# Kernel tuning notes

Hardware: AMD Instinct MI355X
Metric: run time of the kernel (lower is better)

Reference implementation:

```python
import jax, jax.numpy as jnp
import numpy as np

LN_EPS = 1e-5

def _layernorm(x):
    # LayerNorm over last dim, no affine params (elementwise_affine=False)
    mu = jnp.mean(x, axis=-1, keepdims=True)
    var = jnp.var(x, axis=-1, keepdims=True)
    return (x - mu) / jnp.sqrt(var + LN_EPS)

def setup_inputs() -> dict:
    key = jax.random.key(0)
    k1, k2 = jax.random.split(key)
    B, S, D_IN, D_OUT = 4, 2048, 4096, 4096
    x = jax.random.normal(k1, (B, S, D_IN), dtype=jnp.float32)
    # kaiming-uniform-ish init scale (exact distribution irrelevant for correctness baseline)
    bound = 1.0 / np.sqrt(D_IN)
    weight = jax.random.uniform(k2, (D_OUT, D_IN), dtype=jnp.float32, minval=-bound, maxval=bound)
    return {"x": x, "weight": weight}

def reference(x, weight):
    # weight mean-centering and scalar scale beta
    w_centered = weight - jnp.mean(weight)
    beta = jnp.mean(jnp.abs(w_centered))
    x_norm = _layernorm(x)
    w_bin = jnp.sign(w_centered)                       # [D_out, D_in] in {-1,0,+1}
    out = jnp.einsum('bsi,oi->bso', x_norm, w_bin)     # dense GEMM on binarized weights
    return out * beta
```

## Files before the change

### kernel.cpp

```cpp
#include <hip/hip_runtime.h>
#include <hip/hip_bf16.h>
#include <stdint.h>


typedef __bf16 bf16x8 __attribute__((ext_vector_type(8)));
typedef float f32x4 __attribute__((ext_vector_type(4)));

#define BM 128
#define BN 128
#define BK 32


__device__ __forceinline__ void gl_lds16(const void* g, void* l) {
  __builtin_amdgcn_global_load_lds(
      (const __attribute__((address_space(1))) void*)g,
      (__attribute__((address_space(3))) void*)l,
      16, 0, 0);
}

__device__ __forceinline__ unsigned short f2bf_rne(float f) {
  unsigned int u = __float_as_uint(f);
  unsigned int r = (u + 0x7FFFu + ((u >> 16) & 1u)) >> 16;
  return (unsigned short)r;
}

__device__ __forceinline__ float wave_red(float v) {
#pragma unroll
  for (int o = 32; o > 0; o >>= 1) v += __shfl_down(v, o, 64);
  return v;
}

__device__ __forceinline__ float block_red(float v) {
  __shared__ float tmp[4];
  const int wave = threadIdx.x >> 6, lane = threadIdx.x & 63;
  v = wave_red(v);
  if (lane == 0) tmp[wave] = v;
  __syncthreads();
  float r = 0.f;
  if (threadIdx.x == 0) r = tmp[0] + tmp[1] + tmp[2] + tmp[3];
  return r;
}


__global__ void zero_kernel(float* p) {
  if (threadIdx.x < 8) p[threadIdx.x] = 0.f;
}

__global__ __launch_bounds__(256) void wsum_kernel(const float* __restrict__ w,
                                                   float* __restrict__ scal, int n4) {
  int idx = blockIdx.x * 256 + threadIdx.x;
  int stride = gridDim.x * 256;
  const float4* w4 = (const float4*)w;
  float s = 0.f;
  for (int i = idx; i < n4; i += stride) {
    float4 a = w4[i];
    s += a.x + a.y + a.z + a.w;
  }
  float tot = block_red(s);
  if (threadIdx.x == 0) atomicAdd(&scal[0], tot);
}

__global__ __launch_bounds__(256) void wbin_kernel(const float* __restrict__ w,
                                                   float* __restrict__ scal,
                                                   unsigned short* __restrict__ wb,
                                                   int n4, float inv_n) {
  const float mean = scal[0] * inv_n;
  int idx = blockIdx.x * 256 + threadIdx.x;
  int stride = gridDim.x * 256;
  const float4* w4 = (const float4*)w;
  ushort4* wb4 = (ushort4*)wb;
  float sa = 0.f;
  for (int i = idx; i < n4; i += stride) {
    float4 a = w4[i];
    float dx = a.x - mean, dy = a.y - mean, dz = a.z - mean, dw = a.w - mean;
    sa += fabsf(dx) + fabsf(dy) + fabsf(dz) + fabsf(dw);
    ushort4 o;
    o.x = dx > 0.f ? 0x3F80u : (dx < 0.f ? 0xBF80u : 0u);
    o.y = dy > 0.f ? 0x3F80u : (dy < 0.f ? 0xBF80u : 0u);
    o.z = dz > 0.f ? 0x3F80u : (dz < 0.f ? 0xBF80u : 0u);
    o.w = dw > 0.f ? 0x3F80u : (dw < 0.f ? 0xBF80u : 0u);
    wb4[i] = o;
  }
  float tot = block_red(sa);
  if (threadIdx.x == 0) atomicAdd(&scal[1], tot);
}

__global__ __launch_bounds__(256) void ln_kernel(const float* __restrict__ x,
                                                 __bf16* __restrict__ xn) {
  const int row = blockIdx.x;
  const float4* xr = (const float4*)(x + (size_t)row * 4096);
  const int tid = threadIdx.x;
  float4 v[4];
  float s = 0.f, ss = 0.f;
#pragma unroll
  for (int t = 0; t < 4; t++) {
    float4 a = xr[t * 256 + tid];
    v[t] = a;
    s += a.x + a.y + a.z + a.w;
    ss += a.x * a.x + a.y * a.y + a.z * a.z + a.w * a.w;
  }
#pragma unroll
  for (int o = 32; o > 0; o >>= 1) {
    s += __shfl_down(s, o, 64);
    ss += __shfl_down(ss, o, 64);
  }
  __shared__ float rs[8];
  const int wave = tid >> 6, lane = tid & 63;
  if (lane == 0) { rs[wave] = s; rs[4 + wave] = ss; }
  __syncthreads();
  s = rs[0] + rs[1] + rs[2] + rs[3];
  ss = rs[4] + rs[5] + rs[6] + rs[7];
  const float mu = s * (1.0f / 4096.0f);
  const float var = ss * (1.0f / 4096.0f) - mu * mu;
  const float rstd = rsqrtf(var + 1e-5f);
  ushort4* xw = (ushort4*)((unsigned short*)xn + (size_t)row * 4096);
#pragma unroll
  for (int t = 0; t < 4; t++) {
    float4 a = v[t];
    ushort4 o;
    o.x = f2bf_rne((a.x - mu) * rstd);
    o.y = f2bf_rne((a.y - mu) * rstd);
    o.z = f2bf_rne((a.z - mu) * rstd);
    o.w = f2bf_rne((a.w - mu) * rstd);
    xw[t * 256 + tid] = o;
  }
}

__global__ __launch_bounds__(256) void gemm_kernel(const __bf16* __restrict__ A,
                                                   const __bf16* __restrict__ Bm,
                                                   float* __restrict__ C,
                                                   const float* __restrict__ scal,
                                                   float beta_scale,
                                                   int M, int N, int K) {
  __shared__ __align__(16) __bf16 sA[BM * BK];
  __shared__ __align__(16) __bf16 sB[BN * BK];

  const int tid = threadIdx.x;
  const int wave = tid >> 6;
  const int lane = tid & 63;

  const int rowBase = blockIdx.x * BM;
  const int colBase = blockIdx.y * BN;

  const float beta = scal[1] * beta_scale;

  const int sRow = lane >> 2;
  const int sCol = (lane & 3) << 3;
  const __bf16* gA = A + (size_t)(rowBase + sRow) * K + sCol;
  const __bf16* gB = Bm + (size_t)(colBase + sRow) * K + sCol;
  const int c0 = wave * 2, c1 = wave * 2 + 1;

  const int wm = (wave >> 1) << 6;
  const int wn = (wave & 1) << 6;
  const int fr = lane & 15;
  const int fk = (lane >> 4) << 3;

  f32x4 acc[4][4];
#pragma unroll
  for (int i = 0; i < 4; i++)
#pragma unroll
    for (int j = 0; j < 4; j++) acc[i][j] = (f32x4){0.f, 0.f, 0.f, 0.f};

  for (int kt = 0; kt < K; kt += BK) {
    gl_lds16(gA + (size_t)c0 * 16 * K + kt, &sA[c0 * 512]);
    gl_lds16(gA + (size_t)c1 * 16 * K + kt, &sA[c1 * 512]);
    gl_lds16(gB + (size_t)c0 * 16 * K + kt, &sB[c0 * 512]);
    gl_lds16(gB + (size_t)c1 * 16 * K + kt, &sB[c1 * 512]);
    __syncthreads();

    bf16x8 af[4], bf[4];
#pragma unroll
    for (int i = 0; i < 4; i++)
      af[i] = *(const bf16x8*)&sA[(wm + i * 16 + fr) * BK + fk];
#pragma unroll
    for (int j = 0; j < 4; j++)
      bf[j] = *(const bf16x8*)&sB[(wn + j * 16 + fr) * BK + fk];
#pragma unroll
    for (int i = 0; i < 4; i++)
#pragma unroll
      for (int j = 0; j < 4; j++)
        acc[i][j] = __builtin_amdgcn_mfma_f32_16x16x32_bf16(af[i], bf[j], acc[i][j], 0, 0, 0);
    __syncthreads();
  }

  const int orow = rowBase + wm + ((lane >> 4) << 2);
  const int ocol = colBase + wn + (lane & 15);
#pragma unroll
  for (int i = 0; i < 4; i++)
#pragma unroll
    for (int j = 0; j < 4; j++)
#pragma unroll
      for (int r = 0; r < 4; r++)
        C[(size_t)(orow + i * 16 + r) * N + (ocol + j * 16)] = acc[i][j][r] * beta;
}


extern "C" void kernel_launch(void* const* d_in, const int* in_sizes, int n_in,
                              void* d_out, int out_size, void* d_ws, size_t ws_size,
                              hipStream_t stream) {
  const float* x = (const float*)d_in[0];
  const float* w = (const float*)d_in[1];
  float* out = (float*)d_out;

  const int K = 4096;
  const int M = in_sizes[0] / K;
  const int N = in_sizes[1] / K;
  const int nw = N * K;
  const float inv_nw = 1.0f / (float)nw;

  char* ws = (char*)d_ws;
  float* scal = (float*)ws;
  __bf16* wbin = (__bf16*)(ws + 256);
  __bf16* xn = (__bf16*)(ws + 256 + (size_t)nw * 2);

  zero_kernel<<<1, 64, 0, stream>>>(scal);
  wsum_kernel<<<1024, 256, 0, stream>>>(w, scal, nw / 4);
  wbin_kernel<<<1024, 256, 0, stream>>>(w, scal, (unsigned short*)wbin, nw / 4, inv_nw);
  ln_kernel<<<M, 256, 0, stream>>>(x, xn);
  dim3 grid(M / BM, N / BN);
  gemm_kernel<<<grid, 256, 0, stream>>>(xn, wbin, out, scal, inv_nw, M, N, K);
}
```

Before: 674.6 us.

## Double GEMM K-tile to 64 with XOR-swizzled LDS layout

Raises the GEMM K-tile from 32 to 64 so each barrier pair covers two MFMA k-steps. This halves the synchronisation count per unit of work. The global-to-LDS load mapping and the fragment reads use an XOR swizzle on 16-byte chunks to avoid LDS bank conflicts at the wider row stride. It also replaces the tiny zero kernel with hipMemsetAsync. The change doubles LDS per block, which may reduce occupancy, and there is still no double buffering.

```diff
diff --git a/kernel.cpp b/kernel.cpp
--- a/kernel.cpp
+++ b/kernel.cpp
@@ -8,7 +8,7 @@
 
 #define BM 128
 #define BN 128
-#define BK 32
+#define BK 64
 
 
 __device__ __forceinline__ void gl_lds16(const void* g, void* l) {
@@ -41,10 +41,6 @@
   return r;
 }
 
-
-__global__ void zero_kernel(float* p) {
-  if (threadIdx.x < 8) p[threadIdx.x] = 0.f;
-}
 
 __global__ __launch_bounds__(256) void wsum_kernel(const float* __restrict__ w,
                                                    float* __restrict__ scal, int n4) {
@@ -144,16 +140,17 @@
 
   const float beta = scal[1] * beta_scale;
 
-  const int sRow = lane >> 2;
-  const int sCol = (lane & 3) << 3;
+  const int sRow = lane >> 3;
+  const int sCol = ((lane & 7) ^ (lane >> 3)) << 3;
   const __bf16* gA = A + (size_t)(rowBase + sRow) * K + sCol;
   const __bf16* gB = Bm + (size_t)(colBase + sRow) * K + sCol;
-  const int c0 = wave * 2, c1 = wave * 2 + 1;
+  const int r0 = wave * 32;
 
   const int wm = (wave >> 1) << 6;
   const int wn = (wave & 1) << 6;
   const int fr = lane & 15;
-  const int fk = (lane >> 4) << 3;
+  const int kq = lane >> 4;
+  const int swz = fr & 7;
 
   f32x4 acc[4][4];
 #pragma unroll
@@ -162,29 +159,36 @@
     for (int j = 0; j < 4; j++) acc[i][j] = (f32x4){0.f, 0.f, 0.f, 0.f};
 
   for (int kt = 0; kt < K; kt += BK) {
-    gl_lds16(gA + (size_t)c0 * 16 * K + kt, &sA[c0 * 512]);
-    gl_lds16(gA + (size_t)c1 * 16 * K + kt, &sA[c1 * 512]);
-    gl_lds16(gB + (size_t)c0 * 16 * K + kt, &sB[c0 * 512]);
-    gl_lds16(gB + (size_t)c1 * 16 * K + kt, &sB[c1 * 512]);
+#pragma unroll
+    for (int h = 0; h < 4; h++) {
+      gl_lds16(gA + (size_t)(r0 + h * 8) * K + kt, &sA[(r0 + h * 8) * BK]);
+      gl_lds16(gB + (size_t)(r0 + h * 8) * K + kt, &sB[(r0 + h * 8) * BK]);
+    }
     __syncthreads();
 
-    bf16x8 af[4], bf[4];
+    bf16x8 af[4][2], bf[4][2];
 #pragma unroll
     for (int i = 0; i < 4; i++)
-      af[i] = *(const bf16x8*)&sA[(wm + i * 16 + fr) * BK + fk];
+#pragma unroll
+      for (int s = 0; s < 2; s++)
+        af[i][s] = *(const bf16x8*)&sA[(wm + i * 16 + fr) * BK + ((((s << 2) | kq) ^ swz) << 3)];
 #pragma unroll
     for (int j = 0; j < 4; j++)
-      bf[j] = *(const bf16x8*)&sB[(wn + j * 16 + fr) * BK + fk];
-#pragma unroll
-    for (int i = 0; i < 4; i++)
-#pragma unroll
-      for (int j = 0; j < 4; j++)
-        acc[i][j] = __builtin_amdgcn_mfma_f32_16x16x32_bf16(af[i], bf[j], acc[i][j], 0, 0, 0);
+#pragma unroll
+      for (int s = 0; s < 2; s++)
+        bf[j][s] = *(const bf16x8*)&sB[(wn + j * 16 + fr) * BK + ((((s << 2) | kq) ^ swz) << 3)];
+#pragma unroll
+    for (int s = 0; s < 2; s++)
+#pragma unroll
+      for (int i = 0; i < 4; i++)
+#pragma unroll
+        for (int j = 0; j < 4; j++)
+          acc[i][j] = __builtin_amdgcn_mfma_f32_16x16x32_bf16(af[i][s], bf[j][s], acc[i][j], 0, 0, 0);
     __syncthreads();
   }
 
-  const int orow = rowBase + wm + ((lane >> 4) << 2);
-  const int ocol = colBase + wn + (lane & 15);
+  const int orow = rowBase + wm + (kq << 2);
+  const int ocol = colBase + wn + fr;
 #pragma unroll
   for (int i = 0; i < 4; i++)
 #pragma unroll
@@ -213,7 +217,7 @@
   __bf16* wbin = (__bf16*)(ws + 256);
   __bf16* xn = (__bf16*)(ws + 256 + (size_t)nw * 2);
 
-  zero_kernel<<<1, 64, 0, stream>>>(scal);
+  hipMemsetAsync(scal, 0, 8 * sizeof(float), stream);
   wsum_kernel<<<1024, 256, 0, stream>>>(w, scal, nw / 4);
   wbin_kernel<<<1024, 256, 0, stream>>>(w, scal, (unsigned short*)wbin, nw / 4, inv_nw);
   ln_kernel<<<M, 256, 0, stream>>>(x, xn);
```

Measured after the change: 690.7 us. +2.4%, slower.
